# Kernel tuning notes

Hardware: AMD Instinct MI355X
Metric: run time of the kernel (lower is better)

## Reference

```python
import jax, jax.numpy as jnp
import numpy as np

IN_FEATURES = 4096
LOCAL_FEATURES = 128
KERNEL_SIZE = 64
STRIDE = 32
FOLD_NUM = (IN_FEATURES - KERNEL_SIZE) // STRIDE + 1  # 127
BATCH = 4096


def setup_inputs() -> dict:
    key = jax.random.key(0)
    kx, kw, kb = jax.random.split(key, 3)
    x = jax.random.normal(kx, (BATCH, IN_FEATURES), dtype=jnp.float32)
    # Per-window linear weights: torch Linear weight is [out, in] = [local_features, kernel_size]
    bound = 1.0 / np.sqrt(KERNEL_SIZE)
    W = jax.random.uniform(kw, (FOLD_NUM, LOCAL_FEATURES, KERNEL_SIZE),
                           dtype=jnp.float32, minval=-bound, maxval=bound)
    b = jax.random.uniform(kb, (FOLD_NUM, LOCAL_FEATURES),
                           dtype=jnp.float32, minval=-bound, maxval=bound)
    return {"x": x, "W": W, "b": b}


def reference(x, W, b) -> jnp.ndarray:
    # Unfold: windows[f, k] = x[:, f*stride + k] -> [B, FOLD_NUM, KERNEL_SIZE]
    idx = jnp.arange(FOLD_NUM)[:, None] * STRIDE + jnp.arange(KERNEL_SIZE)[None, :]
    windows = x[:, idx]  # [B, F, K]
    # Batched per-window linear: out[b, f, l] = sum_k windows[b,f,k] * W[f,l,k] + b[f,l]
    out = jnp.einsum('bfk,flk->bfl', windows, W) + b[None, :, :]
    # torch.cat along dim 1 over fold index == reshape [B, F*L]
    return out.reshape(x.shape[0], FOLD_NUM * LOCAL_FEATURES)
```

## Files before the change

kernel.cpp:

```cpp
#include <hip/hip_runtime.h>
#include <hip/hip_bf16.h>

#define IN_F 4096
#define LOCAL_F 128
#define KSZ 64
#define STRIDE_ 32
#define FOLDS 127
#define BATCH_ 4096
#define OUT_F (FOLDS * LOCAL_F)
#define WN (FOLDS * LOCAL_F * KSZ)
#define XN (BATCH_ * IN_F)

typedef __attribute__((ext_vector_type(8))) short bf16x8;
typedef __attribute__((ext_vector_type(8))) unsigned short u16x8;
typedef __attribute__((ext_vector_type(4))) float f32x4;

__device__ __forceinline__ unsigned short f2bf(float f) {
    unsigned u = __builtin_bit_cast(unsigned, f);
    u += 0x7fffu + ((u >> 16) & 1u);
    return (unsigned short)(u >> 16);
}

__global__ __launch_bounds__(256)
void cvt_kernel(const float* __restrict__ src, unsigned short* __restrict__ dst, int n) {
    int i = (blockIdx.x * 256 + threadIdx.x) * 8;
    if (i >= n) return;
    float4 a = *reinterpret_cast<const float4*>(src + i);
    float4 c = *reinterpret_cast<const float4*>(src + i + 4);
    u16x8 s;
    s[0] = f2bf(a.x); s[1] = f2bf(a.y); s[2] = f2bf(a.z); s[3] = f2bf(a.w);
    s[4] = f2bf(c.x); s[5] = f2bf(c.y); s[6] = f2bf(c.z); s[7] = f2bf(c.w);
    *reinterpret_cast<u16x8*>(dst + i) = s;
}

__global__ __launch_bounds__(256, 3)
void ll_main(const unsigned short* __restrict__ xbf,
             const unsigned short* __restrict__ Wbf,
             const float* __restrict__ b,
             float* __restrict__ out) {
    const int bg = blockIdx.x;
    const int fg = blockIdx.y;
    const int row0 = bg * 64;

    const int wave = threadIdx.x >> 6;
    const int lane = threadIdx.x & 63;
    const int fold = wave >> 1;
    const int h    = wave & 1;
    const int f = fg * 2 + fold;
    if (f >= FOLDS) return;

    const int l16 = lane & 15;
    const int g   = lane >> 4;

    const unsigned short* Wf = Wbf + ((size_t)f * LOCAL_F + h * 64) * KSZ;
    const unsigned short* xw = xbf + (size_t)row0 * IN_F + f * STRIDE_;

    bf16x8 wf[2][4], af[2][4];
    #pragma unroll
    for (int ks = 0; ks < 2; ++ks) {
        #pragma unroll
        for (int nt = 0; nt < 4; ++nt)
            wf[ks][nt] = *reinterpret_cast<const bf16x8*>(Wf + (nt * 16 + l16) * KSZ + ks * 32 + g * 8);
        #pragma unroll
        for (int mt = 0; mt < 4; ++mt)
            af[ks][mt] = *reinterpret_cast<const bf16x8*>(xw + (size_t)(mt * 16 + l16) * IN_F + ks * 32 + g * 8);
    }

    f32x4 acc[4][4];
    #pragma unroll
    for (int mt = 0; mt < 4; ++mt)
        #pragma unroll
        for (int nt = 0; nt < 4; ++nt)
            acc[mt][nt] = (f32x4){0.f, 0.f, 0.f, 0.f};

    #pragma unroll
    for (int ks = 0; ks < 2; ++ks)
        #pragma unroll
        for (int mt = 0; mt < 4; ++mt)
            #pragma unroll
            for (int nt = 0; nt < 4; ++nt)
                acc[mt][nt] = __builtin_amdgcn_mfma_f32_16x16x32_bf16(wf[ks][nt], af[ks][mt], acc[mt][nt], 0, 0, 0);

    f32x4 bv[4];
    #pragma unroll
    for (int nt = 0; nt < 4; ++nt)
        bv[nt] = *reinterpret_cast<const f32x4*>(b + (size_t)f * LOCAL_F + h * 64 + nt * 16 + 4 * g);

    #pragma unroll
    for (int mt = 0; mt < 4; ++mt) {
        float* orow = out + (size_t)(row0 + mt * 16 + l16) * OUT_F + f * LOCAL_F + h * 64 + 4 * g;
        #pragma unroll
        for (int nt = 0; nt < 4; ++nt) {
            f32x4 v = acc[mt][nt] + bv[nt];
            __builtin_nontemporal_store(v, reinterpret_cast<f32x4*>(orow + nt * 16));
        }
    }
}

extern "C" void kernel_launch(void* const* d_in, const int* in_sizes, int n_in,
                              void* d_out, int out_size, void* d_ws, size_t ws_size,
                              hipStream_t stream) {
    const float* x = (const float*)d_in[0];
    const float* W = (const float*)d_in[1];
    const float* b = (const float*)d_in[2];
    float* out = (float*)d_out;

    unsigned short* xbf = (unsigned short*)d_ws;
    unsigned short* Wbf = (unsigned short*)d_ws + XN;

    cvt_kernel<<<(XN / 8 + 255) / 256, 256, 0, stream>>>(x, xbf, XN);
    cvt_kernel<<<(WN / 8 + 255) / 256, 256, 0, stream>>>(W, Wbf, WN);

    dim3 grid(BATCH_ / 64, 64);
    ll_main<<<grid, 256, 0, stream>>>(xbf, Wbf, b, out);
}
```

Before: 110.6 us.

## Fuse x bf16 conversion into main kernel and retile over 16 rows by 32 folds

Drops the separate pass that converted all of x to bf16; the main kernel now loads fp32 x directly and converts in registers, which removes a full read and write of a 64MB-scale buffer. The work split changes to 16 rows per block with each wave looping over up to 8 folds and covering all 128 outputs, and occupancy is raised to 4. In exchange, W tiles are reloaded once per 16-row block instead of once per 64 rows, and the output stores are now regular rather than nontemporal.

```diff
diff --git a/kernel.cpp b/kernel.cpp
--- a/kernel.cpp
+++ b/kernel.cpp
@@ -9,7 +9,6 @@
 #define BATCH_ 4096
 #define OUT_F (FOLDS * LOCAL_F)
 #define WN (FOLDS * LOCAL_F * KSZ)
-#define XN (BATCH_ * IN_F)
 
 typedef __attribute__((ext_vector_type(8))) short bf16x8;
 typedef __attribute__((ext_vector_type(8))) unsigned short u16x8;
@@ -22,77 +21,74 @@
 }
 
 __global__ __launch_bounds__(256)
-void cvt_kernel(const float* __restrict__ src, unsigned short* __restrict__ dst, int n) {
+void wprep_kernel(const float* __restrict__ W, unsigned short* __restrict__ Wbf) {
     int i = (blockIdx.x * 256 + threadIdx.x) * 8;
-    if (i >= n) return;
-    float4 a = *reinterpret_cast<const float4*>(src + i);
-    float4 c = *reinterpret_cast<const float4*>(src + i + 4);
+    if (i >= WN) return;
+    float4 a = *reinterpret_cast<const float4*>(W + i);
+    float4 c = *reinterpret_cast<const float4*>(W + i + 4);
     u16x8 s;
     s[0] = f2bf(a.x); s[1] = f2bf(a.y); s[2] = f2bf(a.z); s[3] = f2bf(a.w);
     s[4] = f2bf(c.x); s[5] = f2bf(c.y); s[6] = f2bf(c.z); s[7] = f2bf(c.w);
-    *reinterpret_cast<u16x8*>(dst + i) = s;
+    *reinterpret_cast<u16x8*>(Wbf + i) = s;
 }
 
-__global__ __launch_bounds__(256, 3)
-void ll_main(const unsigned short* __restrict__ xbf,
+__global__ __launch_bounds__(256, 4)
+void ll_main(const float* __restrict__ x,
              const unsigned short* __restrict__ Wbf,
              const float* __restrict__ b,
              float* __restrict__ out) {
-    const int bg = blockIdx.x;
-    const int fg = blockIdx.y;
-    const int row0 = bg * 64;
+    const int rg = blockIdx.x;
+    const int fq = blockIdx.y;
+    const int row0 = rg * 16;
 
     const int wave = threadIdx.x >> 6;
     const int lane = threadIdx.x & 63;
-    const int fold = wave >> 1;
-    const int h    = wave & 1;
-    const int f = fg * 2 + fold;
-    if (f >= FOLDS) return;
-
     const int l16 = lane & 15;
     const int g   = lane >> 4;
 
-    const unsigned short* Wf = Wbf + ((size_t)f * LOCAL_F + h * 64) * KSZ;
-    const unsigned short* xw = xbf + (size_t)row0 * IN_F + f * STRIDE_;
-
-    bf16x8 wf[2][4], af[2][4];
-    #pragma unroll
-    for (int ks = 0; ks < 2; ++ks) {
-        #pragma unroll
-        for (int nt = 0; nt < 4; ++nt)
-            wf[ks][nt] = *reinterpret_cast<const bf16x8*>(Wf + (nt * 16 + l16) * KSZ + ks * 32 + g * 8);
-        #pragma unroll
-        for (int mt = 0; mt < 4; ++mt)
-            af[ks][mt] = *reinterpret_cast<const bf16x8*>(xw + (size_t)(mt * 16 + l16) * IN_F + ks * 32 + g * 8);
-    }
-
-    f32x4 acc[4][4];
-    #pragma unroll
-    for (int mt = 0; mt < 4; ++mt)
-        #pragma unroll
-        for (int nt = 0; nt < 4; ++nt)
-            acc[mt][nt] = (f32x4){0.f, 0.f, 0.f, 0.f};
+    const float* xrow = x + (size_t)(row0 + l16) * IN_F;
+    float*       orow = out + (size_t)(row0 + l16) * OUT_F;
 
     #pragma unroll
-    for (int ks = 0; ks < 2; ++ks)
+    for (int j = 0; j < 8; ++j) {
+        const int f = fq * 32 + wave + 4 * j;
+        if (f >= FOLDS) break;
+
+        bf16x8 af[2];
         #pragma unroll
-        for (int mt = 0; mt < 4; ++mt)
+        for (int ks = 0; ks < 2; ++ks) {
+            const float* p = xrow + f * STRIDE_ + ks * 32 + g * 8;
+            float4 a = *reinterpret_cast<const float4*>(p);
+            float4 c = *reinterpret_cast<const float4*>(p + 4);
+            bf16x8 t;
+            t[0] = (short)f2bf(a.x); t[1] = (short)f2bf(a.y);
+            t[2] = (short)f2bf(a.z); t[3] = (short)f2bf(a.w);
+            t[4] = (short)f2bf(c.x); t[5] = (short)f2bf(c.y);
+            t[6] = (short)f2bf(c.z); t[7] = (short)f2bf(c.w);
+            af[ks] = t;
+        }
+
+        f32x4 acc[8];
+        #pragma unroll
+        for (int nt = 0; nt < 8; ++nt) acc[nt] = (f32x4){0.f, 0.f, 0.f, 0.f};
+
+        const unsigned short* Wf = Wbf + (size_t)f * (LOCAL_F * KSZ);
+        #pragma unroll
+        for (int ks = 0; ks < 2; ++ks) {
+            bf16x8 wf[8];
             #pragma unroll
-            for (int nt = 0; nt < 4; ++nt)
-                acc[mt][nt] = __builtin_amdgcn_mfma_f32_16x16x32_bf16(wf[ks][nt], af[ks][mt], acc[mt][nt], 0, 0, 0);
+            for (int nt = 0; nt < 8; ++nt)
+                wf[nt] = *reinterpret_cast<const bf16x8*>(Wf + (nt * 16 + l16) * KSZ + ks * 32 + g * 8);
+            #pragma unroll
+            for (int nt = 0; nt < 8; ++nt)
+                acc[nt] = __builtin_amdgcn_mfma_f32_16x16x32_bf16(wf[nt], af[ks], acc[nt], 0, 0, 0);
+        }
 
-    f32x4 bv[4];
-    #pragma unroll
-    for (int nt = 0; nt < 4; ++nt)
-        bv[nt] = *reinterpret_cast<const f32x4*>(b + (size_t)f * LOCAL_F + h * 64 + nt * 16 + 4 * g);
-
-    #pragma unroll
-    for (int mt = 0; mt < 4; ++mt) {
-        float* orow = out + (size_t)(row0 + mt * 16 + l16) * OUT_F + f * LOCAL_F + h * 64 + 4 * g;
         #pragma unroll
-        for (int nt = 0; nt < 4; ++nt) {
-            f32x4 v = acc[mt][nt] + bv[nt];
-            __builtin_nontemporal_store(v, reinterpret_cast<f32x4*>(orow + nt * 16));
+        for (int nt = 0; nt < 8; ++nt) {
+            f32x4 bv = *reinterpret_cast<const f32x4*>(b + (size_t)f * LOCAL_F + nt * 16 + 4 * g);
+            f32x4 v = acc[nt] + bv;
+            *reinterpret_cast<f32x4*>(orow + (size_t)f * LOCAL_F + nt * 16 + 4 * g) = v;
         }
     }
 }
@@ -104,13 +100,9 @@
     const float* W = (const float*)d_in[1];
     const float* b = (const float*)d_in[2];
     float* out = (float*)d_out;
+    unsigned short* Wbf = (unsigned short*)d_ws;
 
-    unsigned short* xbf = (unsigned short*)d_ws;
-    unsigned short* Wbf = (unsigned short*)d_ws + XN;
-
-    cvt_kernel<<<(XN / 8 + 255) / 256, 256, 0, stream>>>(x, xbf, XN);
-    cvt_kernel<<<(WN / 8 + 255) / 256, 256, 0, stream>>>(W, Wbf, WN);
-
-    dim3 grid(BATCH_ / 64, 64);
-    ll_main<<<grid, 256, 0, stream>>>(xbf, Wbf, b, out);
+    wprep_kernel<<<(WN / 8 + 255) / 256, 256, 0, stream>>>(W, Wbf);
+    dim3 grid(BATCH_ / 16, 4);
+    ll_main<<<grid, 256, 0, stream>>>(x, Wbf, b, out);
 }
```

New measurement: 165.1 us. +49.4%, slower.
